# Kernel tuning notes

Hardware: AMD Instinct MI355X
Metric: run time of the kernel (lower is better)

## Reference

```python
import jax, jax.numpy as jnp
import numpy as np

N = 100000   # nodes
E = 1600000  # edges (avg degree 16)
IN, HID, OUT = 128, 128, 64


def setup_inputs() -> dict:
    key = jax.random.key(0)
    k = jax.random.split(key, 6)
    feat = jax.random.normal(k[0], (N, IN), dtype=jnp.float32)
    src = jax.random.randint(k[1], (E,), 0, N)
    dst = jax.random.randint(k[2], (E,), 0, N)
    W1 = jax.random.normal(k[3], (IN, HID), dtype=jnp.float32) * (1.0 / np.sqrt(IN))
    b1 = jnp.zeros((HID,), dtype=jnp.float32)
    W2 = jax.random.normal(k[4], (HID, OUT), dtype=jnp.float32) * (1.0 / np.sqrt(HID))
    b2 = jnp.zeros((OUT,), dtype=jnp.float32)
    return {"feat": feat, "src": src, "dst": dst, "W1": W1, "b1": b1, "W2": W2, "b2": b2}


def _graph_conv(x, src, dst, c_src, c_dst, W, b):
    # DGL GraphConv, norm='both': D_dst^{-1/2} A (D_src^{-1/2} X W) + b
    # Apply W before the edge gather (mathematically identical, less edge traffic).
    h = (x * c_src[:, None]) @ W                      # [N, out]
    m = jax.ops.segment_sum(h[src], dst, num_segments=N)  # SpMM aggregate
    return m * c_dst[:, None] + b


def reference(feat, src, dst, W1, b1, W2, b2):
    ones = jnp.ones((src.shape[0],), dtype=feat.dtype)
    out_deg = jax.ops.segment_sum(ones, src, num_segments=N)
    in_deg = jax.ops.segment_sum(ones, dst, num_segments=N)
    c_src = jnp.clip(out_deg, 1.0, None) ** -0.5
    c_dst = jnp.clip(in_deg, 1.0, None) ** -0.5
    h = jax.nn.relu(_graph_conv(feat, src, dst, c_src, c_dst, W1, b1))
    h = _graph_conv(h, src, dst, c_src, c_dst, W2, b2)
    # dgl.mean_nodes over a single graph -> [1, OUT]
    return jnp.mean(h, axis=0, keepdims=True)
```

## Files before the change

kernel.cpp:

```cpp
#include <hip/hip_runtime.h>
#include <hip/hip_bf16.h>

#define FD 128
#define OD 64
#define SLOT 64
#define MAXNB 512
#define CHUNK 4096
#define NSLAB 64

typedef __hip_bfloat16 bf16;
typedef unsigned int u32;
typedef unsigned short u16;
typedef unsigned char u8;
typedef __attribute__((ext_vector_type(8))) short short8;
typedef __attribute__((ext_vector_type(4))) float f32x4;
typedef __attribute__((ext_vector_type(2))) float f32x2;

__device__ __forceinline__ float ldf(const float* p, size_t i) { return p[i]; }
__device__ __forceinline__ float ldf(const bf16* p, size_t i) { return __bfloat162float(p[i]); }
__device__ __forceinline__ float us2f(u16 u) {
    union { float f; u32 i; } w; w.i = ((u32)u) << 16; return w.f;
}
__device__ __forceinline__ u16 f2us(float f) {
    bf16 h = __float2bfloat16(f);
    return *reinterpret_cast<u16*>(&h);
}

__device__ __forceinline__ u32 f8e(float x) {
    union { float f; u32 i; } w; w.f = x;
    u32 s = (w.i >> 24) & 0x80u;
    float a = fabsf(x);
    if (a < 0.015625f) {
        u32 m = (u32)(int)rintf(a * 512.0f);
        return s | m;
    }
    if (a > 448.0f) a = 448.0f;
    w.f = a;
    u32 mag = w.i + 0x7FFFFu + ((w.i >> 20) & 1u);
    if (mag > 0x43E00000u) mag = 0x43E00000u;
    u32 e8 = (mag >> 23) - 120u;
    u32 m3 = (mag >> 20) & 7u;
    return s | (e8 << 3) | m3;
}
__device__ __forceinline__ float f8d(u32 b) {
    float v;
    if ((b & 0x78u) == 0u) {
        v = (float)(b & 7u) * 0x1p-9f;
    } else {
        union { u32 i; float f; } w;
        w.i = ((b & 0x7Fu) << 20) + 0x3C000000u;
        v = w.f;
    }
    return (b & 0x80u) ? -v : v;
}

__device__ __forceinline__ u32 sniff(const u16* __restrict__ w1raw, u32* shflag) {
    if (threadIdx.x < 64) {
        int insane = 0;
        for (int i = threadIdx.x; i < 128; i += 64) {
            unsigned e = (w1raw[i] >> 7) & 0xFF;
            if (e != 0 && (e < 100 || e > 140)) insane++;
        }
        for (int o = 32; o > 0; o >>= 1) insane += __shfl_down(insane, o);
        if (threadIdx.x == 0) *shflag = (insane > 16) ? 1u : 0u;
    }
    __syncthreads();
    return *shflag;
}

__global__ __launch_bounds__(1024) void k_hw(const int* __restrict__ src,
                                             const int* __restrict__ dst,
                                             const u16* __restrict__ w1raw,
                                             const void* __restrict__ W1, const void* __restrict__ b1,
                                             u16* __restrict__ W1T, float* __restrict__ b1f,
                                             u32* __restrict__ cmT_d, u32* __restrict__ cmT_s,
                                             int E, int NB) {
    __shared__ u32 smem[1024];
    __shared__ u32 flsh;
    int t = threadIdx.x, blk = blockIdx.x, G = gridDim.x;
    u32 fl = sniff(w1raw, &flsh);

    for (long i = (long)blk * 1024 + t; i < FD * FD; i += (long)G * 1024) {
        int nn = (int)(i >> 7), k = (int)(i & 127);
        W1T[i] = fl ? f2us(ldf((const float*)W1, (size_t)k * FD + nn))
                    : f2us(ldf((const bf16*)W1, (size_t)k * FD + nn));
    }
    if (blk == 0 && t < FD)
        b1f[t] = fl ? ldf((const float*)b1, t) : ldf((const bf16*)b1, t);

    u32* hd = smem;
    u32* hs = smem + 512;
    for (int i = t; i < NB; i += 1024) { hd[i] = 0; hs[i] = 0; }
    __syncthreads();
    long e0 = (long)blk * CHUNK;
    #pragma unroll
    for (int k = 0; k < CHUNK / 1024; k++) {
        long e = e0 + t + 1024L * k;
        if (e < E) {
            atomicAdd(&hd[((u32)dst[e]) >> 8], 1u);
            atomicAdd(&hs[((u32)src[e]) >> 8], 1u);
        }
    }
    __syncthreads();
    for (int i = t; i < NB; i += 1024) {
        cmT_d[(size_t)blk * NB + i] = hd[i];
        cmT_s[(size_t)blk * NB + i] = hs[i];
    }
}

__global__ __launch_bounds__(1024) void k_colpre(u32* __restrict__ cmT_d, u32* __restrict__ cmT_s,
                                                 u32* __restrict__ totd, u32* __restrict__ tots,
                                                 float* __restrict__ accum_slab,
                                                 int NB, int nchunk) {
    __shared__ u32 sS[1024];
    int bb = blockIdx.x, t = threadIdx.x;
    for (long i = (long)bb * 1024 + t; i < NSLAB * FD; i += (long)gridDim.x * 1024)
        accum_slab[i] = 0.0f;
    u32* cm  = (bb < NB) ? cmT_d : cmT_s;
    u32* tot = (bb < NB) ? totd : tots;
    int b = (bb < NB) ? bb : bb - NB;
    u32 carry = 0;
    for (int c0 = 0; c0 < nchunk; c0 += 1024) {
        int c = c0 + t;
        u32 v = (c < nchunk) ? cm[(size_t)c * NB + b] : 0u;
        sS[t] = v;
        __syncthreads();
        for (int o = 1; o < 1024; o <<= 1) {
            u32 x = (t >= o) ? sS[t - o] : 0u;
            __syncthreads();
            sS[t] += x;
            __syncthreads();
        }
        if (c < nchunk) cm[(size_t)c * NB + b] = carry + sS[t] - v;
        u32 bt = sS[1023];
        __syncthreads();
        carry += bt;
    }
    if (t == 0) tot[b] = carry;
}

__global__ __launch_bounds__(1024) void k_scat(const int* __restrict__ src,
                                               const int* __restrict__ dst,
                                               const u32* __restrict__ cmT_d,
                                               const u32* __restrict__ cmT_s,
                                               const u32* __restrict__ totd,
                                               const u32* __restrict__ tots,
                                               u32* __restrict__ bstart_d, u32* __restrict__ bstart_s,
                                               u32* __restrict__ pairs, u32* __restrict__ srcb,
                                               int E, int NB) {
    __shared__ u32 hd[MAXNB], hs[MAXNB];
    __shared__ u32 bD[MAXNB], bS[MAXNB];
    __shared__ u32 sS[MAXNB];
    int t = threadIdx.x, blk = blockIdx.x;

    u32 v = (t < NB) ? totd[t] : 0u;
    if (t < MAXNB) sS[t] = v;
    __syncthreads();
    for (int o = 1; o < MAXNB; o <<= 1) {
        u32 x = (t >= o && t < MAXNB) ? sS[t - o] : 0u;
        __syncthreads();
        if (t < MAXNB) sS[t] += x;
        __syncthreads();
    }
    if (t < NB) bD[t] = sS[t] - v;
    __syncthreads();
    u32 v2 = (t < NB) ? tots[t] : 0u;
    if (t < MAXNB) sS[t] = v2;
    __syncthreads();
    for (int o = 1; o < MAXNB; o <<= 1) {
        u32 x = (t >= o && t < MAXNB) ? sS[t - o] : 0u;
        __syncthreads();
        if (t < MAXNB) sS[t] += x;
        __syncthreads();
    }
    if (t < NB) bS[t] = sS[t] - v2;
    if (blk == 0 && t < NB) { bstart_d[t] = bD[t]; bstart_s[t] = bS[t]; }
    __syncthreads();

    for (int i = t; i < NB; i += 1024) {
        hd[i] = 0; hs[i] = 0;
        bD[i] += cmT_d[(size_t)blk * NB + i];
        bS[i] += cmT_s[(size_t)blk * NB + i];
    }
    __syncthreads();
    long e0 = (long)blk * CHUNK;
    #pragma unroll
    for (int k = 0; k < CHUNK / 1024; k++) {
        long e = e0 + t + 1024L * k;
        if (e < E) {
            u32 s = (u32)src[e], d = (u32)dst[e];
            u32 rd = atomicAdd(&hd[d >> 8], 1u);
            u32 rs = atomicAdd(&hs[s >> 8], 1u);
            pairs[bD[d >> 8] + rd] = ((d & 255u) << 24) | s;
            srcb [bS[s >> 8] + rs] = ((s & 255u) << 24) | d;
        }
    }
}

__global__ __launch_bounds__(1024) void k_csrcs(const u32* __restrict__ pairs,
                                                const u32* __restrict__ srcb,
                                                const u32* __restrict__ bstart_d,
                                                const u32* __restrict__ bstart_s,
                                                const u32* __restrict__ totd,
                                                const u32* __restrict__ tots,
                                                u32* __restrict__ col,
                                                u32* __restrict__ cnt_d, float* __restrict__ c_dst,
                                                float* __restrict__ c_src, int N, int NB) {
    __shared__ u32 lc[256];
    int b0 = blockIdx.x, t = threadIdx.x;
    if (t < 256) lc[t] = 0;
    __syncthreads();
    if (b0 < NB) {
        int b = b0;
        u32 s0 = bstart_d[b], c = totd[b];
        for (u32 i = t; i < c; i += 1024) {
            u32 pk = pairs[s0 + i];
            u32 local = pk >> 24;
            u32 r = atomicAdd(&lc[local], 1u);
            if (r < SLOT) col[(((size_t)b * 256 + local) << 6) + r] = pk & 0xFFFFFFu;
        }
        __syncthreads();
        if (t < 256) {
            int node = b * 256 + t;
            if (node < N) {
                cnt_d[node] = lc[t];
                c_dst[node] = rsqrtf(fmaxf((float)lc[t], 1.0f));
            }
        }
    } else {
        int b = b0 - NB;
        u32 s0 = bstart_s[b], c = tots[b];
        for (u32 i = t; i < c; i += 1024)
            atomicAdd(&lc[srcb[s0 + i] >> 24], 1u);
        __syncthreads();
        if (t < 256) {
            int node = b * 256 + t;
            if (node < N) c_src[node] = rsqrtf(fmaxf((float)lc[t], 1.0f));
        }
    }
}

__global__ __launch_bounds__(1024) void k_wf8(const u32* __restrict__ srcb,
                                              const u32* __restrict__ bstart_s,
                                              const u32* __restrict__ tots,
                                              const float* __restrict__ c_dst,
                                              const float* __restrict__ c_src,
                                              float* __restrict__ wprod,
                                              const u16* __restrict__ w1raw,
                                              const void* __restrict__ feat,
                                              u32* __restrict__ f8w, int N, int NB) {
    int b0 = blockIdx.x, t = threadIdx.x;
    if (b0 < NB) {
        __shared__ float accF[256];
        int b = b0;
        if (t < 256) accF[t] = 0.0f;
        __syncthreads();
        u32 s0 = bstart_s[b], c = tots[b];
        for (u32 i = t; i < c; i += 1024) {
            u32 pk = srcb[s0 + i];
            atomicAdd(&accF[pk >> 24], c_dst[pk & 0xFFFFFFu]);
        }
        __syncthreads();
        if (t < 256) {
            int node = b * 256 + t;
            if (node < N) wprod[node] = accF[t] * c_src[node];
        }
    } else {
        __shared__ float csl[256];
        __shared__ u32 flsh;
        u32 fl = sniff(w1raw, &flsh);
        int b = b0 - NB;
        if (t < 256) {
            int node = b * 256 + t;
            csl[t] = (node < N) ? c_src[node] : 0.0f;
        }
        __syncthreads();
        for (int wi = t; wi < 256 * 32; wi += 1024) {
            int row = wi >> 5;
            int node = b * 256 + row;
            if (node >= N) continue;
            float cs = csl[row];
            size_t p0 = (size_t)node * FD + (size_t)(wi & 31) * 4;
            u32 pk;
            if (fl == 0u) {
                const bf16* f = (const bf16*)feat;
                pk = f8e(cs * ldf(f, p0))       | (f8e(cs * ldf(f, p0 + 1)) << 8)
                   | (f8e(cs * ldf(f, p0 + 2)) << 16) | (f8e(cs * ldf(f, p0 + 3)) << 24);
            } else {
                const float* f = (const float*)feat;
                pk = f8e(cs * ldf(f, p0))       | (f8e(cs * ldf(f, p0 + 1)) << 8)
                   | (f8e(cs * ldf(f, p0 + 2)) << 16) | (f8e(cs * ldf(f, p0 + 3)) << 24);
            }
            f8w[(size_t)node * 32 + (wi & 31)] = pk;
        }
        if (b == 0 && t < 32) f8w[(size_t)N * 32 + t] = 0u;
    }
}

__global__ __launch_bounds__(256) void k_layer1a(const u8* __restrict__ f8,
                                                 const u16* __restrict__ W1T,
                                                 const float* __restrict__ b1f,
                                                 const float* __restrict__ c_dst,
                                                 const unsigned* __restrict__ cnt_d,
                                                 const unsigned* __restrict__ col,
                                                 const float* __restrict__ wprod,
                                                 float* __restrict__ accum_slab, int n) {
    __shared__ __align__(16) u16 xsb[64 * 144];
    __shared__ float b1l[FD];
    __shared__ float cdl[64], wpl[64];
    __shared__ unsigned degl[64];
    int t = threadIdx.x;
    int base = blockIdx.x * 64;

    if (t < FD) b1l[t] = b1f[t];
    if (t < 64) {
        int rr = base + t;
        unsigned cd = (rr < n) ? cnt_d[rr] : 0u;
        cdl[t] = (rr < n) ? c_dst[rr] : 0.0f;
        wpl[t] = (rr < n) ? wprod[rr] : 0.0f;
        degl[t] = (cd < SLOT) ? cd : SLOT;
    }
    __syncthreads();

    int w = __builtin_amdgcn_readfirstlane(t >> 6);
    int l = t & 63;
    int m0 = w * 16;
    int q = l >> 4, lm = l & 15;
    int j0 = l * 2;
    unsigned zrow = (unsigned)n;

    for (int g = 0; g < 16; g++) {
        int loc = m0 + g;
        int node = base + loc;
        unsigned degv = degl[loc];
        size_t cb = ((size_t)node) << 6;
        float acc0 = 0.0f, acc1 = 0.0f;
        for (unsigned qq = 0; qq < degv; qq += 16) {
            unsigned lim = degv - qq;
            const unsigned* cp = col + cb + qq;
            uint4 P0 = *(const uint4*)(cp);
            uint4 P1 = *(const uint4*)(cp + 4);
            uint4 P2 = *(const uint4*)(cp + 8);
            uint4 P3 = *(const uint4*)(cp + 12);
            unsigned raw[16] = {P0.x, P0.y, P0.z, P0.w, P1.x, P1.y, P1.z, P1.w,
                                P2.x, P2.y, P2.z, P2.w, P3.x, P3.y, P3.z, P3.w};
            #pragma unroll
            for (int k = 0; k < 16; k++) {
                unsigned sk = __builtin_amdgcn_readfirstlane(raw[k]);
                sk = ((unsigned)k < lim) ? sk : zrow;
                u32 v = (u32)*(const u16*)(f8 + (((size_t)sk) << 7) + j0);
#if __has_builtin(__builtin_amdgcn_cvt_pk_f32_fp8)
                f32x2 dd = __builtin_amdgcn_cvt_pk_f32_fp8((int)v, false);
                acc0 += dd[0];
                acc1 += dd[1];
#else
                acc0 += f8d(v & 0xFFu);
                acc1 += f8d(v >> 8);
#endif
            }
        }
        u32 pk = ((u32)f2us(acc1) << 16) | (u32)f2us(acc0);
        *(u32*)&xsb[loc * 144 + j0] = pk;
    }

    short8 af[4];
    #pragma unroll
    for (int s = 0; s < 4; s++)
        af[s] = *(const short8*)&xsb[(m0 + lm) * 144 + s * 32 + q * 8];
    __syncthreads();
    float* part = (float*)xsb;

    #pragma unroll 1
    for (int h2 = 0; h2 < 2; h2++) {
        #pragma unroll 1
        for (int tt = 0; tt < 4; tt++) {
            int nglob = h2 * 64 + tt * 16 + lm;
            f32x4 c = {0.0f, 0.0f, 0.0f, 0.0f};
            #pragma unroll
            for (int s = 0; s < 4; s++) {
                short8 bfr = *(const short8*)&W1T[(size_t)nglob * FD + s * 32 + q * 8];
                c = __builtin_amdgcn_mfma_f32_16x16x32_bf16(af[s], bfr, c, 0, 0, 0);
            }
            float bb = b1l[nglob];
            float ps = 0.0f;
            #pragma unroll
            for (int r = 0; r < 4; r++) {
                int loc = m0 + q * 4 + r;
                float hv = fmaxf(c[r] * cdl[loc] + bb, 0.0f);
                ps += wpl[loc] * hv;
            }
            ps += __shfl_down(ps, 32);
            ps += __shfl_down(ps, 16);
            if (l < 16) part[w * FD + nglob] = ps;
        }
    }
    __syncthreads();
    if (t < FD) {
        float v = part[0 * FD + t] + part[1 * FD + t] + part[2 * FD + t] + part[3 * FD + t];
        unsafeAtomicAdd(&accum_slab[(blockIdx.x & (NSLAB - 1)) * FD + t], v);
    }
}

__global__ void k_finalF(const u16* __restrict__ w1raw,
                         const float* __restrict__ accum_slab,
                         const void* __restrict__ W2, const void* __restrict__ b2v,
                         void* __restrict__ out, float invN) {
    __shared__ float a128[FD];
    __shared__ u32 flsh;
    u32 fl = sniff(w1raw, &flsh);
    int t = threadIdx.x;
    float s = 0.0f;
    for (int r = 0; r < NSLAB; r++) s += accum_slab[r * FD + t];
    a128[t] = s;
    __syncthreads();
    if (t < OD) {
        float acc = 0.0f;
        if (fl == 0u) {
            const bf16* w = (const bf16*)W2;
            for (int k = 0; k < FD; k++) acc += a128[k] * ldf(w, (size_t)k * OD + t);
            ((bf16*)out)[t] = __float2bfloat16(acc * invN + ldf((const bf16*)b2v, t));
        } else {
            const float* w = (const float*)W2;
            for (int k = 0; k < FD; k++) acc += a128[k] * ldf(w, (size_t)k * OD + t);
            ((float*)out)[t] = acc * invN + ldf((const float*)b2v, t);
        }
    }
}

extern "C" void kernel_launch(void* const* d_in, const int* in_sizes, int n_in,
                              void* d_out, int out_size, void* d_ws, size_t ws_size,
                              hipStream_t stream) {
    const int* src = (const int*)d_in[1];
    const int* dst = (const int*)d_in[2];
    int N = in_sizes[0] / FD;
    int E = in_sizes[1];
    int NB = (N + 255) >> 8;
    int nchunk = (E + CHUNK - 1) / CHUNK;

    char* ws = (char*)d_ws;
    size_t o = 0;
    auto take = [&](size_t bytes) { size_t r = o; o = (o + bytes + 255) & ~(size_t)255; return r; };
    float*    accum_slab = (float*) (ws + take((size_t)NSLAB * FD * 4));
    u32*      totd     = (u32*)     (ws + take((size_t)NB * 4));
    u32*      tots     = (u32*)     (ws + take((size_t)NB * 4));
    u32*      bstart_d = (u32*)     (ws + take((size_t)NB * 4));
    u32*      bstart_s = (u32*)     (ws + take((size_t)NB * 4));
    float*    wprod    = (float*)   (ws + take((size_t)N * 4));
    float*    c_src    = (float*)   (ws + take((size_t)N * 4));
    float*    c_dst    = (float*)   (ws + take((size_t)N * 4));
    unsigned* cnt_d    = (unsigned*)(ws + take((size_t)N * 4));
    u16*      W1T      = (u16*)     (ws + take(FD * FD * 2));
    float*    b1f      = (float*)   (ws + take(FD * 4));
    u32*      cmT_d    = (u32*)     (ws + take((size_t)NB * nchunk * 4));
    u32*      cmT_s    = (u32*)     (ws + take((size_t)NB * nchunk * 4));
    u32*      pairs    = (u32*)     (ws + take((size_t)E * 4));
    u32*      srcb     = (u32*)     (ws + take((size_t)E * 4));
    u32*      col      = (u32*)     (ws + take((size_t)N * SLOT * 4));
    u8*       f8       = (u8*)      (ws + take(((size_t)N + 1) * FD));

    const u16* w1raw = (const u16*)d_in[3];

    k_hw<<<nchunk, 1024, 0, stream>>>(src, dst, w1raw, d_in[3], d_in[4], W1T, b1f,
                                      cmT_d, cmT_s, E, NB);
    k_colpre<<<2 * NB, 1024, 0, stream>>>(cmT_d, cmT_s, totd, tots, accum_slab, NB, nchunk);
    k_scat<<<nchunk, 1024, 0, stream>>>(src, dst, cmT_d, cmT_s, totd, tots,
                                        bstart_d, bstart_s, pairs, srcb, E, NB);
    k_csrcs<<<2 * NB, 1024, 0, stream>>>(pairs, srcb, bstart_d, bstart_s, totd, tots,
                                         col, cnt_d, c_dst, c_src, N, NB);
    k_wf8<<<2 * NB, 1024, 0, stream>>>(srcb, bstart_s, tots, c_dst, c_src, wprod,
                                       w1raw, d_in[0], (u32*)f8, N, NB);

    int gl1 = (N + 63) / 64;
    k_layer1a<<<gl1, 256, 0, stream>>>(f8, W1T, b1f, c_dst, cnt_d, col, wprod, accum_slab, N);

    float invN = 1.0f / (float)N;
    k_finalF<<<1, 128, 0, stream>>>(w1raw, accum_slab, d_in[5], d_in[6], d_out, invN);
}
```

Baseline: 238.6 us.

## Fuse fp8 feature quantization into CSR build, pair node gathers, enlarge chunk

Moves the fp8 quantization of the scaled features into the source-degree half of k_csrcs, so c_src is used directly from registers and one launch-level dependency is removed. The wprod reduction becomes its own smaller kernel. The layer-1 gather now processes two destination nodes at once to expose more independent loads. The edge-bucketing CHUNK is doubled, which halves the number of chunk blocks. Together these trade fewer launches and more memory-level parallelism for higher register pressure and longer per-block work.

```diff
diff --git a/kernel.cpp b/kernel.cpp
--- a/kernel.cpp
+++ b/kernel.cpp
@@ -5,7 +5,7 @@
 #define OD 64
 #define SLOT 64
 #define MAXNB 512
-#define CHUNK 4096
+#define CHUNK 8192
 #define NSLAB 64
 
 typedef __hip_bfloat16 bf16;
@@ -205,7 +205,10 @@
                                                 const u32* __restrict__ tots,
                                                 u32* __restrict__ col,
                                                 u32* __restrict__ cnt_d, float* __restrict__ c_dst,
-                                                float* __restrict__ c_src, int N, int NB) {
+                                                float* __restrict__ c_src,
+                                                const u16* __restrict__ w1raw,
+                                                const void* __restrict__ feat,
+                                                u32* __restrict__ f8w, int N, int NB) {
     __shared__ u32 lc[256];
     int b0 = blockIdx.x, t = threadIdx.x;
     if (t < 256) lc[t] = 0;
@@ -228,6 +231,9 @@
             }
         }
     } else {
+        __shared__ float csl[256];
+        __shared__ u32 flsh;
+        u32 fl = sniff(w1raw, &flsh);
         int b = b0 - NB;
         u32 s0 = bstart_s[b], c = tots[b];
         for (u32 i = t; i < c; i += 1024)
@@ -235,44 +241,12 @@
         __syncthreads();
         if (t < 256) {
             int node = b * 256 + t;
-            if (node < N) c_src[node] = rsqrtf(fmaxf((float)lc[t], 1.0f));
-        }
-    }
-}
-
-__global__ __launch_bounds__(1024) void k_wf8(const u32* __restrict__ srcb,
-                                              const u32* __restrict__ bstart_s,
-                                              const u32* __restrict__ tots,
-                                              const float* __restrict__ c_dst,
-                                              const float* __restrict__ c_src,
-                                              float* __restrict__ wprod,
-                                              const u16* __restrict__ w1raw,
-                                              const void* __restrict__ feat,
-                                              u32* __restrict__ f8w, int N, int NB) {
-    int b0 = blockIdx.x, t = threadIdx.x;
-    if (b0 < NB) {
-        __shared__ float accF[256];
-        int b = b0;
-        if (t < 256) accF[t] = 0.0f;
-        __syncthreads();
-        u32 s0 = bstart_s[b], c = tots[b];
-        for (u32 i = t; i < c; i += 1024) {
-            u32 pk = srcb[s0 + i];
-            atomicAdd(&accF[pk >> 24], c_dst[pk & 0xFFFFFFu]);
-        }
-        __syncthreads();
-        if (t < 256) {
-            int node = b * 256 + t;
-            if (node < N) wprod[node] = accF[t] * c_src[node];
-        }
-    } else {
-        __shared__ float csl[256];
-        __shared__ u32 flsh;
-        u32 fl = sniff(w1raw, &flsh);
-        int b = b0 - NB;
-        if (t < 256) {
-            int node = b * 256 + t;
-            csl[t] = (node < N) ? c_src[node] : 0.0f;
+            float cs = 0.0f;
+            if (node < N) {
+                cs = rsqrtf(fmaxf((float)lc[t], 1.0f));
+                c_src[node] = cs;
+            }
+            csl[t] = cs;
         }
         __syncthreads();
         for (int wi = t; wi < 256 * 32; wi += 1024) {
@@ -297,6 +271,28 @@
     }
 }
 
+__global__ __launch_bounds__(1024) void k_wprod(const u32* __restrict__ srcb,
+                                                const u32* __restrict__ bstart_s,
+                                                const u32* __restrict__ tots,
+                                                const float* __restrict__ c_dst,
+                                                const float* __restrict__ c_src,
+                                                float* __restrict__ wprod, int N) {
+    __shared__ float accF[256];
+    int b = blockIdx.x, t = threadIdx.x;
+    if (t < 256) accF[t] = 0.0f;
+    __syncthreads();
+    u32 s0 = bstart_s[b], c = tots[b];
+    for (u32 i = t; i < c; i += 1024) {
+        u32 pk = srcb[s0 + i];
+        atomicAdd(&accF[pk >> 24], c_dst[pk & 0xFFFFFFu]);
+    }
+    __syncthreads();
+    if (t < 256) {
+        int node = b * 256 + t;
+        if (node < N) wprod[node] = accF[t] * c_src[node];
+    }
+}
+
 __global__ __launch_bounds__(256) void k_layer1a(const u8* __restrict__ f8,
                                                  const u16* __restrict__ W1T,
                                                  const float* __restrict__ b1f,
@@ -329,38 +325,51 @@
     int j0 = l * 2;
     unsigned zrow = (unsigned)n;
 
-    for (int g = 0; g < 16; g++) {
-        int loc = m0 + g;
-        int node = base + loc;
-        unsigned degv = degl[loc];
-        size_t cb = ((size_t)node) << 6;
-        float acc0 = 0.0f, acc1 = 0.0f;
-        for (unsigned qq = 0; qq < degv; qq += 16) {
-            unsigned lim = degv - qq;
-            const unsigned* cp = col + cb + qq;
-            uint4 P0 = *(const uint4*)(cp);
-            uint4 P1 = *(const uint4*)(cp + 4);
-            uint4 P2 = *(const uint4*)(cp + 8);
-            uint4 P3 = *(const uint4*)(cp + 12);
-            unsigned raw[16] = {P0.x, P0.y, P0.z, P0.w, P1.x, P1.y, P1.z, P1.w,
-                                P2.x, P2.y, P2.z, P2.w, P3.x, P3.y, P3.z, P3.w};
+    for (int g = 0; g < 16; g += 2) {
+        int locA = m0 + g, locB = m0 + g + 1;
+        unsigned degA = degl[locA], degB = degl[locB];
+        size_t cbA = ((size_t)(base + locA)) << 6;
+        size_t cbB = ((size_t)(base + locB)) << 6;
+        float a0A = 0.0f, a1A = 0.0f, a0B = 0.0f, a1B = 0.0f;
+        unsigned nbA = (degA + 15u) >> 4, nbB = (degB + 15u) >> 4;
+        unsigned nb = nbA > nbB ? nbA : nbB;
+        for (unsigned bb = 0; bb < nb; bb++) {
+            unsigned qq = bb * 16u;
+            const unsigned* cpA = col + cbA + qq;
+            const unsigned* cpB = col + cbB + qq;
+            uint4 A0 = *(const uint4*)(cpA),     A1 = *(const uint4*)(cpA + 4);
+            uint4 A2 = *(const uint4*)(cpA + 8), A3 = *(const uint4*)(cpA + 12);
+            uint4 B0 = *(const uint4*)(cpB),     B1 = *(const uint4*)(cpB + 4);
+            uint4 B2 = *(const uint4*)(cpB + 8), B3 = *(const uint4*)(cpB + 12);
+            int limA = (int)degA - (int)qq;
+            int limB = (int)degB - (int)qq;
+            unsigned rawA[16] = {A0.x, A0.y, A0.z, A0.w, A1.x, A1.y, A1.z, A1.w,
+                                 A2.x, A2.y, A2.z, A2.w, A3.x, A3.y, A3.z, A3.w};
+            unsigned rawB[16] = {B0.x, B0.y, B0.z, B0.w, B1.x, B1.y, B1.z, B1.w,
+                                 B2.x, B2.y, B2.z, B2.w, B3.x, B3.y, B3.z, B3.w};
             #pragma unroll
             for (int k = 0; k < 16; k++) {
-                unsigned sk = __builtin_amdgcn_readfirstlane(raw[k]);
-                sk = ((unsigned)k < lim) ? sk : zrow;
-                u32 v = (u32)*(const u16*)(f8 + (((size_t)sk) << 7) + j0);
+                unsigned skA = __builtin_amdgcn_readfirstlane(rawA[k]);
+                unsigned skB = __builtin_amdgcn_readfirstlane(rawB[k]);
+                skA = (k < limA) ? skA : zrow;
+                skB = (k < limB) ? skB : zrow;
+                u32 vA = (u32)*(const u16*)(f8 + (((size_t)skA) << 7) + j0);
+                u32 vB = (u32)*(const u16*)(f8 + (((size_t)skB) << 7) + j0);
 #if __has_builtin(__builtin_amdgcn_cvt_pk_f32_fp8)
-                f32x2 dd = __builtin_amdgcn_cvt_pk_f32_fp8((int)v, false);
-                acc0 += dd[0];
-                acc1 += dd[1];
+                f32x2 dA = __builtin_amdgcn_cvt_pk_f32_fp8((int)vA, false);
+                f32x2 dB = __builtin_amdgcn_cvt_pk_f32_fp8((int)vB, false);
+                a0A += dA[0]; a1A += dA[1];
+                a0B += dB[0]; a1B += dB[1];
 #else
-                acc0 += f8d(v & 0xFFu);
-                acc1 += f8d(v >> 8);
+                a0A += f8d(vA & 0xFFu); a1A += f8d(vA >> 8);
+                a0B += f8d(vB & 0xFFu); a1B += f8d(vB >> 8);
 #endif
             }
         }
-        u32 pk = ((u32)f2us(acc1) << 16) | (u32)f2us(acc0);
-        *(u32*)&xsb[loc * 144 + j0] = pk;
+        u32 pkA = ((u32)f2us(a1A) << 16) | (u32)f2us(a0A);
+        u32 pkB = ((u32)f2us(a1B) << 16) | (u32)f2us(a0B);
+        *(u32*)&xsb[locA * 144 + j0] = pkA;
+        *(u32*)&xsb[locB * 144 + j0] = pkB;
     }
 
     short8 af[4];
@@ -466,9 +475,9 @@
     k_scat<<<nchunk, 1024, 0, stream>>>(src, dst, cmT_d, cmT_s, totd, tots,
                                         bstart_d, bstart_s, pairs, srcb, E, NB);
     k_csrcs<<<2 * NB, 1024, 0, stream>>>(pairs, srcb, bstart_d, bstart_s, totd, tots,
-                                         col, cnt_d, c_dst, c_src, N, NB);
-    k_wf8<<<2 * NB, 1024, 0, stream>>>(srcb, bstart_s, tots, c_dst, c_src, wprod,
-                                       w1raw, d_in[0], (u32*)f8, N, NB);
+                                         col, cnt_d, c_dst, c_src, w1raw, d_in[0],
+                                         (u32*)f8, N, NB);
+    k_wprod<<<NB, 1024, 0, stream>>>(srcb, bstart_s, tots, c_dst, c_src, wprod, N);
 
     int gl1 = (N + 63) / 64;
     k_layer1a<<<gl1, 256, 0, stream>>>(f8, W1T, b1f, c_dst, cnt_d, col, wprod, accum_slab, N);
```

Result: no change. 238.6 us (-0.0%).
